# Optimization experiments

Measured on AMD Instinct MI355X. Metric: run time of the kernel, lower is better.

Reference implementation:

```python
import jax, jax.numpy as jnp
import numpy as np

EPS = 1e-5
B, H, W = 128, 98, 40

def _conv2d(x, w):
    return jax.lax.conv_general_dilated(x, w, (1, 1), 'VALID', dimension_numbers=('NCHW', 'OIHW', 'NCHW'))

def _bn_ch(x, g, b):
    # BatchNorm over (B,H,W) per channel (training-mode batch stats, as in the torch default mode)
    m = jnp.mean(x, (0, 2, 3), keepdims=True)
    v = jnp.var(x, (0, 2, 3), keepdims=True)
    return (x - m) * jax.lax.rsqrt(v + EPS) * g[None, :, None, None] + b[None, :, None, None]

def _bn_all(x, g, b):
    # BatchNorm3d(1): single channel -> normalize over the whole tensor
    m = jnp.mean(x)
    v = jnp.var(x)
    return (x - m) * jax.lax.rsqrt(v + EPS) * g[0] + b[0]

def _lc(h, w, b):
    # 62 distinct tiny Conv3d(1,1,(3,1,1)) == locally-connected window-3 conv over channel axis: 64 -> 62
    out = b[None, :, None, None]
    for k in range(3):
        out = out + h[:, k:k + 62] * w[None, :, k, None, None]
    return out

def _lc_block(h, lcw, lcb, gs, bs, Wm, bm, gm, bbm):
    h = jax.nn.relu(_bn_all(_lc(h, lcw, lcb), gs, bs))
    # Conv3d kernel (62,1,1): pure channel mixing 62 -> 64 (no relu after, matching torch code)
    h = jnp.einsum('bdhw,cd->bchw', h, Wm) + bm[None, :, None, None]
    return _bn_ch(h, gm, bbm)

def setup_inputs():
    ks = iter(jax.random.split(jax.random.key(0), 64))
    def rn(shape, s=0.05):
        return jax.random.normal(next(ks), shape, jnp.float32) * s
    d = {}
    d['x'] = jax.random.normal(next(ks), (B, H * 0 + 98 if False else 1, 98, 40), jnp.float32) if False else jax.random.normal(next(ks), (B, 1, H, W), jnp.float32)
    d['W11'] = rn((64, 1, 20, 8)); d['b11'] = rn((64,)); d['g11'] = jnp.ones((64,), jnp.float32); d['be11'] = jnp.zeros((64,), jnp.float32)
    d['lc1_w'] = rn((62, 3), 0.3); d['lc1_b'] = rn((62,)); d['g12'] = jnp.ones((1,), jnp.float32); d['be12'] = jnp.zeros((1,), jnp.float32)
    d['W13'] = rn((64, 62)); d['b13'] = rn((64,)); d['g13'] = jnp.ones((64,), jnp.float32); d['be13'] = jnp.zeros((64,), jnp.float32)
    d['W21'] = rn((64, 64, 15, 8), 0.01); d['b21'] = rn((64,)); d['g21'] = jnp.ones((64,), jnp.float32); d['be21'] = jnp.zeros((64,), jnp.float32)
    d['lc2_w'] = rn((62, 3), 0.3); d['lc2_b'] = rn((62,)); d['g22'] = jnp.ones((1,), jnp.float32); d['be22'] = jnp.zeros((1,), jnp.float32)
    d['W23'] = rn((64, 62)); d['b23'] = rn((64,)); d['g23'] = jnp.ones((64,), jnp.float32); d['be23'] = jnp.zeros((64,), jnp.float32)
    d['W31'] = rn((64, 64, 10, 8), 0.01); d['b31'] = rn((64,)); d['g31'] = jnp.ones((64,), jnp.float32); d['be31'] = jnp.zeros((64,), jnp.float32)
    d['lc3_w'] = rn((62, 3), 0.3); d['lc3_b'] = rn((62,)); d['g32'] = jnp.ones((1,), jnp.float32); d['be32'] = jnp.zeros((1,), jnp.float32)
    d['W33'] = rn((64, 62)); d['b33'] = rn((64,)); d['g33'] = jnp.ones((64,), jnp.float32); d['be33'] = jnp.zeros((64,), jnp.float32)
    d['Wf1'] = rn((64, 64 * 56 * 19), 0.01); d['bf1'] = rn((64,)); d['gf'] = jnp.ones((64,), jnp.float32); d['bef'] = jnp.zeros((64,), jnp.float32)
    d['Wf2'] = rn((35, 64)); d['bf2'] = rn((35,))
    return d

def reference(x, W11, b11, g11, be11, lc1_w, lc1_b, g12, be12, W13, b13, g13, be13, W21, b21, g21, be21, lc2_w, lc2_b, g22, be22, W23, b23, g23, be23, W31, b31, g31, be31, lc3_w, lc3_b, g32, be32, W33, b33, g33, be33, Wf1, bf1, gf, bef, Wf2, bf2):
    h = jax.nn.relu(_bn_ch(_conv2d(x, W11) + b11[None, :, None, None], g11, be11))      # [B,64,79,33]
    h = _lc_block(h, lc1_w, lc1_b, g12, be12, W13, b13, g13, be13)                       # [B,64,79,33]
    h = jax.nn.relu(_bn_ch(_conv2d(h, W21) + b21[None, :, None, None], g21, be21))       # [B,64,65,26]
    h = _lc_block(h, lc2_w, lc2_b, g22, be22, W23, b23, g23, be23)                       # [B,64,65,26]
    h = jax.nn.relu(_bn_ch(_conv2d(h, W31) + b31[None, :, None, None], g31, be31))       # [B,64,56,19]
    h = _lc_block(h, lc3_w, lc3_b, g32, be32, W33, b33, g33, be33)                       # [B,64,56,19]
    h = h.reshape(h.shape[0], -1)                                                        # [B,68096]
    h = h @ Wf1.T + bf1
    m = jnp.mean(h, 0)
    v = jnp.var(h, 0)
    h = jax.nn.relu((h - m) * jax.lax.rsqrt(v + EPS) * gf + bef)
    return h @ Wf2.T + bf2
```

## Files before the change

kernel.cpp:

```cpp
#include <hip/hip_runtime.h>

typedef __bf16 bfrag __attribute__((ext_vector_type(8)));
typedef float ffrag __attribute__((ext_vector_type(16)));

constexpr int Bn  = 128;
constexpr int H0  = 98, Wi0 = 40;
constexpr int KH1 = 20, KW1 = 8, H1 = 79, Wo1 = 33, P1 = H1 * Wo1;
constexpr int KH2 = 15, KW2 = 8, H2 = 65, Wo2 = 26, P2 = H2 * Wo2;
constexpr int KH3 = 10, KW3 = 8, H3 = 56, Wo3 = 19, P3 = H3 * Wo3;
constexpr int M1  = Bn * P1;
constexpr int M2  = Bn * P2;
constexpr int M3  = Bn * P3;
constexpr int KFC = 64 * P3;
constexpr int FCCH = 128;
constexpr int FCKL = KFC / FCCH;
constexpr float EPSF = 1e-5f;

constexpr size_t oA  = 0;
constexpr size_t oB  = oA  + (size_t)Bn * 64 * P1;
constexpr size_t oW2 = oB  + (size_t)Bn * 62 * P1;
constexpr size_t oW3 = oW2 + 245760;
constexpr size_t oW1 = oW3 + 163840;
constexpr size_t oWM = oW1 + 5120;
constexpr size_t oBF = oWM + 6144;
constexpr size_t oP  = oBF + 128;
constexpr size_t oSt = oP  + (size_t)FCCH * 8192;
constexpr size_t oF  = oSt + 9 * 128;

__device__ __forceinline__ float wred(float v) {
    #pragma unroll
    for (int o = 32; o > 0; o >>= 1) v += __shfl_down(v, o);
    return v;
}

constexpr int NZ  = 9 * 128;
constexpr int NW1 = 10240;
constexpr int NWM = 3 * 4096;
constexpr int NPREP = NZ + NW1 + NWM;
__global__ __launch_bounds__(256) void k_prep_all(
    const float* __restrict__ W11, const float* __restrict__ W13,
    const float* __restrict__ W23, const float* __restrict__ W33,
    __bf16* __restrict__ wq1, __bf16* __restrict__ wqm,
    float* __restrict__ st)
{
    int idx = blockIdx.x * 256 + threadIdx.x;
    if (idx < NZ) { st[idx] = 0.f; return; }
    idx -= NZ;
    if (idx < NW1) {
        int j = idx & 7, oc = (idx >> 3) & 63, khh = idx >> 9;
        wq1[idx] = (__bf16)W11[(size_t)oc * 160 + khh * 8 + j];
        return;
    }
    idx -= NW1;
    if (idx < NWM) {
        int which = idx >> 12, r = idx & 4095;
        int j = r & 7, oc = (r >> 3) & 63, sub = (r >> 9) & 1, ks = r >> 10;
        int k = ks * 16 + sub * 8 + j;
        const float* Wm = which == 0 ? W13 : (which == 1 ? W23 : W33);
        wqm[idx] = (k < 62) ? (__bf16)Wm[oc * 62 + k] : (__bf16)0.f;
    }
}

template <int KH, int KW>
__global__ __launch_bounds__(256) void k_foldw(
    const float* __restrict__ W, const float* __restrict__ stp,
    const float* __restrict__ g, const float* __restrict__ be,
    float inv, const float* __restrict__ bias,
    __bf16* __restrict__ wqf, float* __restrict__ biasf)
{
    constexpr int KK = KH * KW;
    __shared__ float sSc[64], sSh[64], ls[4];
    const int t = threadIdx.x;
    if (t < 64) {
        float mm = stp[t] * inv;
        float vv = stp[64 + t] * inv - mm * mm;
        float sc = g[t] * rsqrtf(vv + EPSF);
        sSc[t] = sc;
        sSh[t] = be[t] - mm * sc;
    }
    __syncthreads();
    const int oc = blockIdx.x;
    float local = 0.f;
    for (int i = t; i < 64 * KK; i += 256) {
        int ic = i / KK, rem = i - ic * KK;
        int kh = rem / KW, kw = rem - kh * KW;
        float wv = W[(((size_t)oc * 64 + ic) * KH + kh) * KW + kw];
        int c = ic >> 4, sub = (ic >> 3) & 1, j = ic & 7, pos = kh * KW + kw;
        wqf[(size_t)pos * 4096 + c * 1024 + sub * 512 + oc * 8 + j] = (__bf16)(wv * sSc[ic]);
        local += wv * sSh[ic];
    }
    local = wred(local);
    int wv2 = t >> 6, ln = t & 63;
    if (ln == 0) ls[wv2] = local;
    __syncthreads();
    if (t == 0) biasf[oc] = bias[oc] + ls[0] + ls[1] + ls[2] + ls[3];
}

constexpr int C1COPY = 1736;
__global__ __launch_bounds__(256, 2) void k_conv1m(
    const float* __restrict__ x, const __bf16* __restrict__ wq,
    const float* __restrict__ bias, float* __restrict__ out,
    float* __restrict__ sto)
{
    const int b = blockIdx.y;
    const int m0 = blockIdx.x * 512;
    const int t = threadIdx.x, lane = t & 63, wv = t >> 6;
    const int l31 = lane & 31, lh = lane >> 5;
    __shared__ __align__(16) __bf16 X8[8 * C1COPY];

    const int oh_lo = m0 / Wo1;
    int abase[4];
    #pragma unroll
    for (int mt = 0; mt < 4; ++mt) {
        int m = m0 + wv * 128 + mt * 32 + l31;
        int mc = m > P1 - 1 ? P1 - 1 : m;
        int oh = mc / Wo1, ow = mc - oh * Wo1;
        int s = ow & 7;
        abase[mt] = s * C1COPY + (oh - oh_lo) * 48 + (ow - s);
    }
    for (int idx = t; idx < 8 * 36 * 6; idx += 256) {
        int s = idx / 216; int rr = idx - s * 216;
        int r = rr / 6, q = rr - r * 6;
        int ih = oh_lo + r; if (ih > H0 - 1) ih = H0 - 1;
        const float* src = x + ((size_t)b * H0 + ih) * Wi0;
        __bf16 tmp[8] __attribute__((aligned(16)));
        #pragma unroll
        for (int j = 0; j < 8; ++j) {
            int col = q * 8 + s + j; if (col > Wi0 - 1) col = Wi0 - 1;
            tmp[j] = (__bf16)src[col];
        }
        *(uint4*)&X8[s * C1COPY + r * 48 + q * 8] = *(uint4*)tmp;
    }
    __syncthreads();

    ffrag acc[4][2] = {};
    #pragma unroll 1
    for (int st2 = 0; st2 < 10; ++st2) {
        const int khl = st2 * 2 + lh;
        const __bf16* wp = wq + ((size_t)khl * 64 + l31) * 8;
        bfrag b0 = *(const bfrag*)(wp);
        bfrag b1 = *(const bfrag*)(wp + 256);
        #pragma unroll
        for (int mt = 0; mt < 4; ++mt) {
            bfrag a = *(const bfrag*)&X8[abase[mt] + khl * 48];
            acc[mt][0] = __builtin_amdgcn_mfma_f32_32x32x16_bf16(a, b0, acc[mt][0], 0, 0, 0);
            acc[mt][1] = __builtin_amdgcn_mfma_f32_32x32x16_bf16(a, b1, acc[mt][1], 0, 0, 0);
        }
    }

    float sS[2] = {0.f, 0.f}, sSS[2] = {0.f, 0.f};
    #pragma unroll
    for (int nt = 0; nt < 2; ++nt) {
        int oc = nt * 32 + l31;
        float bv = bias[oc];
        float* op = out + ((size_t)b * 64 + oc) * P1;
        #pragma unroll
        for (int mt = 0; mt < 4; ++mt) {
            int mbase = m0 + wv * 128 + mt * 32 + lh * 4;
            #pragma unroll
            for (int g = 0; g < 4; ++g) {
                int mr = mbase + g * 8;
                float v0 = acc[mt][nt][g * 4 + 0] + bv;
                float v1 = acc[mt][nt][g * 4 + 1] + bv;
                float v2 = acc[mt][nt][g * 4 + 2] + bv;
                float v3 = acc[mt][nt][g * 4 + 3] + bv;
                if (mr + 1 < P1) {
                    *(float2*)(op + mr) = make_float2(v0, v1);
                    sS[nt] += v0 + v1; sSS[nt] += v0 * v0 + v1 * v1;
                    if (mr + 3 < P1) {
                        *(float2*)(op + mr + 2) = make_float2(v2, v3);
                        sS[nt] += v2 + v3; sSS[nt] += v2 * v2 + v3 * v3;
                    } else if (mr + 2 < P1) {
                        op[mr + 2] = v2; sS[nt] += v2; sSS[nt] += v2 * v2;
                    }
                } else if (mr < P1) {
                    op[mr] = v0; sS[nt] += v0; sSS[nt] += v0 * v0;
                }
            }
        }
    }
    #pragma unroll
    for (int nt = 0; nt < 2; ++nt) {
        sS[nt]  += __shfl_down(sS[nt], 32);
        sSS[nt] += __shfl_down(sSS[nt], 32);
    }
    __syncthreads();
    float* redS  = (float*)X8;
    float* redSS = redS + 256;
    if (lane < 32) {
        #pragma unroll
        for (int nt = 0; nt < 2; ++nt) {
            redS[wv * 64 + nt * 32 + l31]  = sS[nt];
            redSS[wv * 64 + nt * 32 + l31] = sSS[nt];
        }
    }
    __syncthreads();
    if (t < 64) {
        atomicAdd(&sto[t],      redS[t] + redS[64 + t] + redS[128 + t] + redS[192 + t]);
        atomicAdd(&sto[64 + t], redSS[t] + redSS[64 + t] + redSS[128 + t] + redSS[192 + t]);
    }
}

template <int POS>
__global__ __launch_bounds__(256) void k_lc(const float* __restrict__ in,
                                            const float* __restrict__ stp,
                                            const float* __restrict__ g,
                                            const float* __restrict__ be,
                                            float inv,
                                            const float* __restrict__ lcw,
                                            const float* __restrict__ lcb,
                                            __bf16* __restrict__ Z,
                                            float* __restrict__ sto) {
    __shared__ float sAff[128];
    __shared__ float sred[4], ssred[4];
    if (threadIdx.x < 64) {
        int tt = threadIdx.x;
        float mm = stp[tt] * inv;
        float vv = stp[64 + tt] * inv - mm * mm;
        float sc = g[tt] * rsqrtf(vv + EPSF);
        sAff[tt] = sc;
        sAff[64 + tt] = be[tt] - mm * sc;
    }
    __syncthreads();
    int morig = blockIdx.x * 256 + threadIdx.x;
    bool valid = morig < Bn * POS;
    int m = valid ? morig : Bn * POS - 1;
    int b = m / POS; int p = m - b * POS;
    const float* ip = in + (size_t)b * 64 * POS + p;
    __bf16 zb[64] __attribute__((aligned(16)));
    zb[62] = (__bf16)0.f; zb[63] = (__bf16)0.f;
    float ts = 0.f, tss = 0.f;
    float y0 = fmaxf(sAff[0] * ip[0]           + sAff[64], 0.f);
    float y1 = fmaxf(sAff[1] * ip[(size_t)POS] + sAff[65], 0.f);
    for (int c = 0; c < 62; ++c) {
        float y2 = fmaxf(sAff[c + 2] * ip[(size_t)(c + 2) * POS] + sAff[64 + c + 2], 0.f);
        float o = lcb[c] + y0 * lcw[c * 3] + y1 * lcw[c * 3 + 1] + y2 * lcw[c * 3 + 2];
        zb[c] = (__bf16)o;
        if (valid) { ts += o; tss += o * o; }
        y0 = y1; y1 = y2;
    }
    __bf16* zp = Z + (size_t)m * 64;
    #pragma unroll
    for (int j = 0; j < 8; ++j)
        *(uint4*)(zp + j * 8) = *(uint4*)(zb + j * 8);
    ts = wred(ts); tss = wred(tss);
    int wv = threadIdx.x >> 6, ln = threadIdx.x & 63;
    if (ln == 0) { sred[wv] = ts; ssred[wv] = tss; }
    __syncthreads();
    if (threadIdx.x == 0) {
        atomicAdd(&sto[0],  sred[0] + sred[1] + sred[2] + sred[3]);
        atomicAdd(&sto[64], ssred[0] + ssred[1] + ssred[2] + ssred[3]);
    }
}

template <int POS, int IH, int IW, bool OUTBF>
__global__ __launch_bounds__(256, 2) void k_mixm(
    const __bf16* __restrict__ Z, const float* __restrict__ stp,
    const float* __restrict__ g, const float* __restrict__ be,
    float inv, const __bf16* __restrict__ wqm,
    const float* __restrict__ bm, void* __restrict__ outv,
    float* __restrict__ sto)
{
    const int b = blockIdx.y;
    const int m0 = blockIdx.x * 512;
    const int t = threadIdx.x, lane = t & 63, wv = t >> 6;
    const int l31 = lane & 31, lh = lane >> 5;

    float mm = stp[0] * inv;
    float vv = stp[64] * inv - mm * mm;
    float s0 = g[0] * rsqrtf(vv + EPSF);
    float t0 = be[0] - mm * s0;

    size_t zbase[4];
    #pragma unroll
    for (int mt = 0; mt < 4; ++mt) {
        int m = m0 + wv * 128 + mt * 32 + l31;
        int mc = m > POS - 1 ? POS - 1 : m;
        zbase[mt] = ((size_t)b * POS + mc) * 64;
    }

    ffrag acc[4][2] = {};
    #pragma unroll
    for (int ks = 0; ks < 4; ++ks) {
        const __bf16* wp = wqm + ks * 1024 + lh * 512 + l31 * 8;
        bfrag b0 = *(const bfrag*)wp;
        bfrag b1 = *(const bfrag*)(wp + 256);
        #pragma unroll
        for (int mt = 0; mt < 4; ++mt) {
            uint4 raw = *(const uint4*)(Z + zbase[mt] + ks * 16 + lh * 8);
            const __bf16* zin = (const __bf16*)&raw;
            __bf16 zout[8] __attribute__((aligned(16)));
            #pragma unroll
            for (int j = 0; j < 8; ++j) {
                float f = (float)zin[j];
                zout[j] = (__bf16)fmaxf(fmaf(s0, f, t0), 0.f);
            }
            bfrag a = *(const bfrag*)zout;
            acc[mt][0] = __builtin_amdgcn_mfma_f32_32x32x16_bf16(a, b0, acc[mt][0], 0, 0, 0);
            acc[mt][1] = __builtin_amdgcn_mfma_f32_32x32x16_bf16(a, b1, acc[mt][1], 0, 0, 0);
        }
    }

    float sS[2] = {0.f, 0.f}, sSS[2] = {0.f, 0.f};
    #pragma unroll
    for (int nt = 0; nt < 2; ++nt) {
        int oc = nt * 32 + l31;
        float bv = bm[oc];
        if constexpr (OUTBF) {
            __bf16* op = (__bf16*)outv;
            #pragma unroll
            for (int mt = 0; mt < 4; ++mt) {
                int mbase = m0 + wv * 128 + mt * 32 + lh * 4;
                #pragma unroll
                for (int g4 = 0; g4 < 4; ++g4) {
                    #pragma unroll
                    for (int q = 0; q < 4; ++q) {
                        int mr = mbase + g4 * 8 + q;
                        if (mr < POS) {
                            float v = acc[mt][nt][g4 * 4 + q] + bv;
                            int ih = mr / IW, iw = mr - ih * IW;
                            op[((size_t)(b * IH + ih) * 2 + nt) * (IW * 32) + iw * 32 + l31] = (__bf16)v;
                            sS[nt] += v; sSS[nt] += v * v;
                        }
                    }
                }
            }
        } else {
            float* op = (float*)outv + ((size_t)b * 64 + oc) * POS;
            #pragma unroll
            for (int mt = 0; mt < 4; ++mt) {
                int mbase = m0 + wv * 128 + mt * 32 + lh * 4;
                #pragma unroll
                for (int g4 = 0; g4 < 4; ++g4) {
                    int mr = mbase + g4 * 8;
                    if (mr < POS) {
                        float v0 = acc[mt][nt][g4 * 4 + 0] + bv;
                        float v1 = acc[mt][nt][g4 * 4 + 1] + bv;
                        *(float2*)(op + mr) = make_float2(v0, v1);
                        sS[nt] += v0 + v1; sSS[nt] += v0 * v0 + v1 * v1;
                        if (mr + 2 < POS) {
                            float v2 = acc[mt][nt][g4 * 4 + 2] + bv;
                            float v3 = acc[mt][nt][g4 * 4 + 3] + bv;
                            *(float2*)(op + mr + 2) = make_float2(v2, v3);
                            sS[nt] += v2 + v3; sSS[nt] += v2 * v2 + v3 * v3;
                        }
                    }
                }
            }
        }
    }
    #pragma unroll
    for (int nt = 0; nt < 2; ++nt) {
        sS[nt]  += __shfl_down(sS[nt], 32);
        sSS[nt] += __shfl_down(sSS[nt], 32);
    }
    __shared__ float red[512];
    if (lane < 32) {
        #pragma unroll
        for (int nt = 0; nt < 2; ++nt) {
            red[wv * 64 + nt * 32 + l31]       = sS[nt];
            red[256 + wv * 64 + nt * 32 + l31] = sSS[nt];
        }
    }
    __syncthreads();
    if (t < 64) {
        atomicAdd(&sto[t],      red[t] + red[64 + t] + red[128 + t] + red[192 + t]);
        atomicAdd(&sto[64 + t], red[256 + t] + red[320 + t] + red[384 + t] + red[448 + t]);
    }
}

template <int KH, int KW, int IH, int IW, int OH, int OW, int NR>
__global__ __launch_bounds__(256, 2) void k_convmfma(
    const __bf16* __restrict__ in,
    const __bf16* __restrict__ wq,
    const float* __restrict__ bias,
    float* __restrict__ out,
    float* __restrict__ sto)
{
    constexpr int P = OH * OW;
    const int b  = blockIdx.y;
    const int m0 = blockIdx.x * 512;
    const int t  = threadIdx.x;
    const int lane = t & 63;
    const int wv = t >> 6;
    const int l31 = lane & 31, lh = lane >> 5;

    __shared__ __align__(16) __bf16 As[NR * IW * 32 + 64];

    const int oh_lo = m0 / OW;
    int posm[4];
    #pragma unroll
    for (int mt = 0; mt < 4; ++mt) {
        int m = m0 + wv * 128 + mt * 32 + l31;
        int mc = m > P - 1 ? P - 1 : m;
        int oh = mc / OW, ow = mc - oh * OW;
        posm[mt] = (oh - oh_lo) * IW + ow;
    }

    ffrag acc[4][2] = {};

    for (int ich = 0; ich < 2; ++ich) {
        __syncthreads();
        constexpr int ROWCH = IW * 4;
        constexpr int CH = NR * ROWCH;
        for (int idx = t; idx < CH; idx += 256) {
            int r = idx / ROWCH, o = idx - r * ROWCH;
            int ih = oh_lo + r; if (ih > IH - 1) ih = IH - 1;
            const __bf16* src = in + ((size_t)(b * IH + ih) * 2 + ich) * (IW * 32) + o * 8;
            int sw = idx ^ ((idx >> 2) & 7);
            *(uint4*)&As[sw * 8] = *(const uint4*)src;
        }
        __syncthreads();

        const __bf16* wich = wq + ich * 2048;
        for (int kh = 0; kh < KH; ++kh) {
            const int rowoff = kh * IW;
            const __bf16* wkh = wich + (size_t)(kh * KW) * 4096 + lh * 512 + l31 * 8;
            #pragma unroll 1
            for (int kw = 0; kw < KW; ++kw) {
                const __bf16* wp = wkh + kw * 4096;
                #pragma unroll
                for (int cc = 0; cc < 2; ++cc) {
                    bfrag b0 = *(const bfrag*)(wp + cc * 1024);
                    bfrag b1 = *(const bfrag*)(wp + cc * 1024 + 256);
                    #pragma unroll
                    for (int mt = 0; mt < 4; ++mt) {
                        int X = posm[mt] + rowoff + kw;
                        int gc = (X << 2) + cc * 2 + lh;
                        bfrag a = *(const bfrag*)&As[(gc ^ (X & 7)) * 8];
                        acc[mt][0] = __builtin_amdgcn_mfma_f32_32x32x16_bf16(a, b0, acc[mt][0], 0, 0, 0);
                        acc[mt][1] = __builtin_amdgcn_mfma_f32_32x32x16_bf16(a, b1, acc[mt][1], 0, 0, 0);
                    }
                }
            }
        }
    }

    float sS[2] = {0.f, 0.f}, sSS[2] = {0.f, 0.f};
    #pragma unroll
    for (int nt = 0; nt < 2; ++nt) {
        int oc = nt * 32 + l31;
        float bv = bias[oc];
        float* op = out + ((size_t)b * 64 + oc) * P;
        #pragma unroll
        for (int mt = 0; mt < 4; ++mt) {
            int mbase = m0 + wv * 128 + mt * 32 + lh * 4;
            #pragma unroll
            for (int g = 0; g < 4; ++g) {
                int mr = mbase + g * 8;
                if (mr < P) {
                    float v0 = acc[mt][nt][g * 4 + 0] + bv;
                    float v1 = acc[mt][nt][g * 4 + 1] + bv;
                    *(float2*)(op + mr) = make_float2(v0, v1);
                    sS[nt] += v0 + v1; sSS[nt] += v0 * v0 + v1 * v1;
                    if (mr + 2 < P) {
                        float v2 = acc[mt][nt][g * 4 + 2] + bv;
                        float v3 = acc[mt][nt][g * 4 + 3] + bv;
                        *(float2*)(op + mr + 2) = make_float2(v2, v3);
                        sS[nt] += v2 + v3; sSS[nt] += v2 * v2 + v3 * v3;
                    }
                }
            }
        }
    }
    #pragma unroll
    for (int nt = 0; nt < 2; ++nt) {
        sS[nt]  += __shfl_down(sS[nt], 32);
        sSS[nt] += __shfl_down(sSS[nt], 32);
    }
    __syncthreads();
    float* redS  = (float*)As;
    float* redSS = redS + 256;
    if (lane < 32) {
        #pragma unroll
        for (int nt = 0; nt < 2; ++nt) {
            redS[wv * 64 + nt * 32 + l31]  = sS[nt];
            redSS[wv * 64 + nt * 32 + l31] = sSS[nt];
        }
    }
    __syncthreads();
    if (t < 64) {
        atomicAdd(&sto[t],      redS[t] + redS[64 + t] + redS[128 + t] + redS[192 + t]);
        atomicAdd(&sto[64 + t], redSS[t] + redSS[64 + t] + redSS[128 + t] + redSS[192 + t]);
    }
}

__global__ __launch_bounds__(256) void k_transpose(const float* __restrict__ in,
                                                   const float* __restrict__ stp,
                                                   const float* __restrict__ g,
                                                   const float* __restrict__ be,
                                                   float inv,
                                                   float* __restrict__ hT) {
    __shared__ float tile[32][33];
    int j0 = blockIdx.x * 32, b0 = blockIdx.y * 32;
    int lo = threadIdx.x & 31, hi = threadIdx.x >> 5;
    int c  = (j0 + lo) / P3;
    float mm = stp[c] * inv;
    float vv = stp[64 + c] * inv - mm * mm;
    float sc = g[c] * rsqrtf(vv + EPSF);
    float sh = be[c] - mm * sc;
    #pragma unroll
    for (int tt = 0; tt < 4; ++tt) {
        int bl = tt * 8 + hi;
        tile[bl][lo] = sc * in[(size_t)(b0 + bl) * KFC + (j0 + lo)] + sh;
    }
    __syncthreads();
    #pragma unroll
    for (int tt = 0; tt < 4; ++tt) {
        int jl = tt * 8 + hi;
        hT[(size_t)(j0 + jl) * Bn + b0 + lo] = tile[lo][jl];
    }
}

__global__ __launch_bounds__(256) void k_fc1(const float* __restrict__ hT,
                                             const float* __restrict__ Wf1,
                                             float* __restrict__ Pb) {
    int lane = threadIdx.x & 63;
    int f0 = __builtin_amdgcn_readfirstlane((threadIdx.x >> 6) * 16);
    int b  = blockIdx.y * 64 + lane;
    int kc = blockIdx.x;
    int k0 = kc * FCKL;
    float acc[16] = {};
    for (int k = k0; k < k0 + FCKL; ++k) {
        float hv = hT[(size_t)k * Bn + b];
        #pragma unroll
        for (int f = 0; f < 16; ++f)
            acc[f] += hv * Wf1[(size_t)(f0 + f) * KFC + k];
    }
    float* pp = Pb + (size_t)kc * 8192 + (size_t)b * 64 + f0;
    #pragma unroll
    for (int f = 0; f < 16; ++f) pp[f] = acc[f];
}

__global__ __launch_bounds__(256) void k_fc1red(const float* __restrict__ Pb,
                                                float* __restrict__ F) {
    int m = blockIdx.x * 256 + threadIdx.x;
    float s = 0.f;
    for (int kc = 0; kc < FCCH; ++kc) s += Pb[(size_t)kc * 8192 + m];
    F[m] = s;
}

__global__ __launch_bounds__(256) void k_fcfin(const float* __restrict__ F,
                                               const float* __restrict__ bf1,
                                               const float* __restrict__ gf,
                                               const float* __restrict__ bef,
                                               const float* __restrict__ Wf2,
                                               const float* __restrict__ bf2,
                                               float* __restrict__ out) {
    __shared__ float sF[8192];
    __shared__ float sfa[128];
    const int t = threadIdx.x;
    for (int m = t; m < 8192; m += 256) sF[m] = F[m];
    __syncthreads();
    if (t < 64) {
        float s = 0.f, ss = 0.f;
        for (int b = 0; b < Bn; ++b) {
            float v = sF[b * 64 + t] + bf1[t];
            s += v; ss += v * v;
        }
        float m  = s / 128.f;
        float va = ss / 128.f - m * m;
        float sc = gf[t] * rsqrtf(va + EPSF);
        sfa[t] = sc;
        sfa[64 + t] = sc * bf1[t] + bef[t] - m * sc;
    }
    __syncthreads();
    for (int m = t; m < Bn * 35; m += 256) {
        int b = m / 35, o = m - b * 35;
        float acc = bf2[o];
        for (int ff = 0; ff < 64; ++ff) {
            int f = (ff + t) & 63;
            float z = fmaxf(sfa[f] * sF[b * 64 + f] + sfa[64 + f], 0.f);
            acc += z * Wf2[o * 64 + f];
        }
        out[m] = acc;
    }
}

extern "C" void kernel_launch(void* const* d_in, const int* in_sizes, int n_in,
                              void* d_out, int out_size, void* d_ws, size_t ws_size,
                              hipStream_t stream) {
    const float* x    = (const float*)d_in[0];
    const float* W11  = (const float*)d_in[1];
    const float* b11  = (const float*)d_in[2];
    const float* g11  = (const float*)d_in[3];
    const float* be11 = (const float*)d_in[4];
    const float* lc1w = (const float*)d_in[5];
    const float* lc1b = (const float*)d_in[6];
    const float* g12  = (const float*)d_in[7];
    const float* be12 = (const float*)d_in[8];
    const float* W13  = (const float*)d_in[9];
    const float* b13  = (const float*)d_in[10];
    const float* g13  = (const float*)d_in[11];
    const float* be13 = (const float*)d_in[12];
    const float* W21  = (const float*)d_in[13];
    const float* b21  = (const float*)d_in[14];
    const float* g21  = (const float*)d_in[15];
    const float* be21 = (const float*)d_in[16];
    const float* lc2w = (const float*)d_in[17];
    const float* lc2b = (const float*)d_in[18];
    const float* g22  = (const float*)d_in[19];
    const float* be22 = (const float*)d_in[20];
    const float* W23  = (const float*)d_in[21];
    const float* b23  = (const float*)d_in[22];
    const float* g23  = (const float*)d_in[23];
    const float* be23 = (const float*)d_in[24];
    const float* W31  = (const float*)d_in[25];
    const float* b31  = (const float*)d_in[26];
    const float* g31  = (const float*)d_in[27];
    const float* be31 = (const float*)d_in[28];
    const float* lc3w = (const float*)d_in[29];
    const float* lc3b = (const float*)d_in[30];
    const float* g32  = (const float*)d_in[31];
    const float* be32 = (const float*)d_in[32];
    const float* W33  = (const float*)d_in[33];
    const float* b33  = (const float*)d_in[34];
    const float* g33  = (const float*)d_in[35];
    const float* be33 = (const float*)d_in[36];
    const float* Wf1  = (const float*)d_in[37];
    const float* bf1  = (const float*)d_in[38];
    const float* gf   = (const float*)d_in[39];
    const float* bef  = (const float*)d_in[40];
    const float* Wf2  = (const float*)d_in[41];
    const float* bf2  = (const float*)d_in[42];

    float* ws  = (float*)d_ws;
    float* A   = ws + oA;
    float* Bb  = ws + oB;
    __bf16* Abf = (__bf16*)(ws + oA);
    __bf16* Bbf = (__bf16*)(ws + oB);
    __bf16* wq2f = (__bf16*)(ws + oW2);
    __bf16* wq3f = (__bf16*)(ws + oW3);
    __bf16* wq1  = (__bf16*)(ws + oW1);
    __bf16* wqm  = (__bf16*)(ws + oWM);
    float* bfold = ws + oBF;
    float* Pb  = ws + oP;
    float* st  = ws + oSt;
    float* F   = ws + oF;

    const int blk1 = (M1 + 255) / 256;
    const int blk2 = M2 / 256;
    const int blk3 = M3 / 256;

    k_prep_all<<<(NPREP + 255) / 256, 256, 0, stream>>>(W11, W13, W23, W33, wq1, wqm, st);

    k_conv1m<<<dim3((P1 + 511) / 512, Bn), 256, 0, stream>>>(x, wq1, b11, A, st + 0 * 128);
    k_lc<P1><<<blk1, 256, 0, stream>>>(A, st + 0 * 128, g11, be11, 1.0f / (float)M1,
                                       lc1w, lc1b, Bbf, st + 1 * 128);
    k_mixm<P1, H1, Wo1, true><<<dim3((P1 + 511) / 512, Bn), 256, 0, stream>>>(
        Bbf, st + 1 * 128, g12, be12, 1.0f / (62.0f * (float)M1),
        wqm + 0 * 4096, b13, (void*)Abf, st + 2 * 128);

    k_foldw<KH2, KW2><<<64, 256, 0, stream>>>(W21, st + 2 * 128, g13, be13,
                                              1.0f / (float)M1, b21, wq2f, bfold + 0);
    k_convmfma<KH2, KW2, H1, Wo1, H2, Wo2, 35>
        <<<dim3((P2 + 511) / 512, Bn), 256, 0, stream>>>(Abf, wq2f, bfold + 0, Bb, st + 3 * 128);
    k_lc<P2><<<blk2, 256, 0, stream>>>(Bb, st + 3 * 128, g21, be21, 1.0f / (float)M2,
                                       lc2w, lc2b, Abf, st + 4 * 128);
    k_mixm<P2, H2, Wo2, true><<<dim3((P2 + 511) / 512, Bn), 256, 0, stream>>>(
        Abf, st + 4 * 128, g22, be22, 1.0f / (62.0f * (float)M2),
        wqm + 1 * 4096, b23, (void*)Bbf, st + 5 * 128);

    k_foldw<KH3, KW3><<<64, 256, 0, stream>>>(W31, st + 5 * 128, g23, be23,
                                              1.0f / (float)M2, b31, wq3f, bfold + 64);
    k_convmfma<KH3, KW3, H2, Wo2, H3, Wo3, 37>
        <<<dim3((P3 + 511) / 512, Bn), 256, 0, stream>>>(Bbf, wq3f, bfold + 64, A, st + 6 * 128);
    k_lc<P3><<<blk3, 256, 0, stream>>>(A, st + 6 * 128, g31, be31, 1.0f / (float)M3,
                                       lc3w, lc3b, Bbf, st + 7 * 128);
    k_mixm<P3, 1, 1, false><<<dim3((P3 + 511) / 512, Bn), 256, 0, stream>>>(
        Bbf, st + 7 * 128, g32, be32, 1.0f / (62.0f * (float)M3),
        wqm + 2 * 4096, b33, (void*)A, st + 8 * 128);

    k_transpose<<<dim3(KFC / 32, Bn / 32), 256, 0, stream>>>(
        A, st + 8 * 128, g33, be33, 1.0f / (float)M3, Bb);
    k_fc1<<<dim3(FCCH, 2), 256, 0, stream>>>(Bb, Wf1, Pb);
    k_fc1red<<<32, 256, 0, stream>>>(Pb, F);
    k_fcfin<<<1, 256, 0, stream>>>(F, bf1, gf, bef, Wf2, bf2, (float*)d_out);
}
```

Measured before the change: 1.068 ms.

## Use bf16 MFMA for FC1, spread BN stat atomics over banks, retile conv3

The scalar fp32 FC1 with its transpose kernel is replaced by a bf16 conversion pass for activations and Wf1, followed by an MFMA-based FC1 split over 112 K-chunks. The per-channel statistics atomics are spread across four banks (and 64 slots for the single-channel LC stats), and readers sum the banks, to reduce atomic contention. The third conv is retuned to 3 M-tiles per wave with smaller blocks, and the kw loop is unrolled by 2. FC1 now uses bf16 inputs, which lowers precision, and a conversion pass over Wf1 is added on every call.

```diff
diff --git a/kernel.cpp b/kernel.cpp
--- a/kernel.cpp
+++ b/kernel.cpp
@@ -12,20 +12,23 @@
 constexpr int M2  = Bn * P2;
 constexpr int M3  = Bn * P3;
 constexpr int KFC = 64 * P3;
-constexpr int FCCH = 128;
+constexpr int FCCH = 112;
 constexpr int FCKL = KFC / FCCH;
+constexpr int FCKS = FCKL / 16;
 constexpr float EPSF = 1e-5f;
 
-constexpr size_t oA  = 0;
-constexpr size_t oB  = oA  + (size_t)Bn * 64 * P1;
-constexpr size_t oW2 = oB  + (size_t)Bn * 62 * P1;
-constexpr size_t oW3 = oW2 + 245760;
-constexpr size_t oW1 = oW3 + 163840;
-constexpr size_t oWM = oW1 + 5120;
-constexpr size_t oBF = oWM + 6144;
-constexpr size_t oP  = oBF + 128;
-constexpr size_t oSt = oP  + (size_t)FCCH * 8192;
-constexpr size_t oF  = oSt + 9 * 128;
+constexpr size_t oA   = 0;
+constexpr size_t oB   = oA  + (size_t)Bn * 64 * P1;
+constexpr size_t oHB  = oB;
+constexpr size_t oWF  = oB  + 4358144;
+constexpr size_t oW2  = oB  + (size_t)Bn * 62 * P1;
+constexpr size_t oW3  = oW2 + 245760;
+constexpr size_t oW1  = oW3 + 163840;
+constexpr size_t oWM  = oW1 + 5120;
+constexpr size_t oBF  = oWM + 6144;
+constexpr size_t oP   = oBF + 128;
+constexpr size_t oSt  = oP  + (size_t)FCCH * 8192;
+constexpr size_t oF   = oSt + 9 * 512;
 
 __device__ __forceinline__ float wred(float v) {
     #pragma unroll
@@ -33,7 +36,11 @@
     return v;
 }
 
-constexpr int NZ  = 9 * 128;
+__device__ __forceinline__ float bank4(const float* stp, int c) {
+    return stp[c] + stp[128 + c] + stp[256 + c] + stp[384 + c];
+}
+
+constexpr int NZ  = 9 * 512;
 constexpr int NW1 = 10240;
 constexpr int NWM = 3 * 4096;
 constexpr int NPREP = NZ + NW1 + NWM;
@@ -72,8 +79,8 @@
     __shared__ float sSc[64], sSh[64], ls[4];
     const int t = threadIdx.x;
     if (t < 64) {
-        float mm = stp[t] * inv;
-        float vv = stp[64 + t] * inv - mm * mm;
+        float mm = bank4(stp, t) * inv;
+        float vv = bank4(stp, 64 + t) * inv - mm * mm;
         float sc = g[t] * rsqrtf(vv + EPSF);
         sSc[t] = sc;
         sSh[t] = be[t] - mm * sc;
@@ -196,8 +203,9 @@
     }
     __syncthreads();
     if (t < 64) {
-        atomicAdd(&sto[t],      redS[t] + redS[64 + t] + redS[128 + t] + redS[192 + t]);
-        atomicAdd(&sto[64 + t], redSS[t] + redSS[64 + t] + redSS[128 + t] + redSS[192 + t]);
+        int bank = ((blockIdx.x ^ blockIdx.y) & 3) * 128;
+        atomicAdd(&sto[bank + t],      redS[t] + redS[64 + t] + redS[128 + t] + redS[192 + t]);
+        atomicAdd(&sto[bank + 64 + t], redSS[t] + redSS[64 + t] + redSS[128 + t] + redSS[192 + t]);
     }
 }
 
@@ -215,8 +223,8 @@
     __shared__ float sred[4], ssred[4];
     if (threadIdx.x < 64) {
         int tt = threadIdx.x;
-        float mm = stp[tt] * inv;
-        float vv = stp[64 + tt] * inv - mm * mm;
+        float mm = bank4(stp, tt) * inv;
+        float vv = bank4(stp, 64 + tt) * inv - mm * mm;
         float sc = g[tt] * rsqrtf(vv + EPSF);
         sAff[tt] = sc;
         sAff[64 + tt] = be[tt] - mm * sc;
@@ -248,8 +256,9 @@
     if (ln == 0) { sred[wv] = ts; ssred[wv] = tss; }
     __syncthreads();
     if (threadIdx.x == 0) {
-        atomicAdd(&sto[0],  sred[0] + sred[1] + sred[2] + sred[3]);
-        atomicAdd(&sto[64], ssred[0] + ssred[1] + ssred[2] + ssred[3]);
+        int slot = blockIdx.x & 63;
+        atomicAdd(&sto[slot],      sred[0] + sred[1] + sred[2] + sred[3]);
+        atomicAdd(&sto[64 + slot], ssred[0] + ssred[1] + ssred[2] + ssred[3]);
     }
 }
 
@@ -266,8 +275,11 @@
     const int t = threadIdx.x, lane = t & 63, wv = t >> 6;
     const int l31 = lane & 31, lh = lane >> 5;
 
-    float mm = stp[0] * inv;
-    float vv = stp[64] * inv - mm * mm;
+    float gs = 0.f, gss = 0.f;
+    #pragma unroll
+    for (int i = 0; i < 64; ++i) { gs += stp[i]; gss += stp[64 + i]; }
+    float mm = gs * inv;
+    float vv = gss * inv - mm * mm;
     float s0 = g[0] * rsqrtf(vv + EPSF);
     float t0 = be[0] - mm * s0;
 
@@ -364,12 +376,13 @@
     }
     __syncthreads();
     if (t < 64) {
-        atomicAdd(&sto[t],      red[t] + red[64 + t] + red[128 + t] + red[192 + t]);
-        atomicAdd(&sto[64 + t], red[256 + t] + red[320 + t] + red[384 + t] + red[448 + t]);
-    }
-}
-
-template <int KH, int KW, int IH, int IW, int OH, int OW, int NR>
+        int bank = ((blockIdx.x ^ blockIdx.y) & 3) * 128;
+        atomicAdd(&sto[bank + t],      red[t] + red[64 + t] + red[128 + t] + red[192 + t]);
+        atomicAdd(&sto[bank + 64 + t], red[256 + t] + red[320 + t] + red[384 + t] + red[448 + t]);
+    }
+}
+
+template <int KH, int KW, int IH, int IW, int OH, int OW, int NR, int MT>
 __global__ __launch_bounds__(256, 2) void k_convmfma(
     const __bf16* __restrict__ in,
     const __bf16* __restrict__ wq,
@@ -378,8 +391,9 @@
     float* __restrict__ sto)
 {
     constexpr int P = OH * OW;
+    constexpr int MB = 128 * MT;
     const int b  = blockIdx.y;
-    const int m0 = blockIdx.x * 512;
+    const int m0 = blockIdx.x * MB;
     const int t  = threadIdx.x;
     const int lane = t & 63;
     const int wv = t >> 6;
@@ -388,16 +402,16 @@
     __shared__ __align__(16) __bf16 As[NR * IW * 32 + 64];
 
     const int oh_lo = m0 / OW;
-    int posm[4];
-    #pragma unroll
-    for (int mt = 0; mt < 4; ++mt) {
-        int m = m0 + wv * 128 + mt * 32 + l31;
+    int posm[MT];
+    #pragma unroll
+    for (int mt = 0; mt < MT; ++mt) {
+        int m = m0 + wv * (32 * MT) + mt * 32 + l31;
         int mc = m > P - 1 ? P - 1 : m;
         int oh = mc / OW, ow = mc - oh * OW;
         posm[mt] = (oh - oh_lo) * IW + ow;
     }
 
-    ffrag acc[4][2] = {};
+    ffrag acc[MT][2] = {};
 
     for (int ich = 0; ich < 2; ++ich) {
         __syncthreads();
@@ -416,7 +430,7 @@
         for (int kh = 0; kh < KH; ++kh) {
             const int rowoff = kh * IW;
             const __bf16* wkh = wich + (size_t)(kh * KW) * 4096 + lh * 512 + l31 * 8;
-            #pragma unroll 1
+            #pragma unroll 2
             for (int kw = 0; kw < KW; ++kw) {
                 const __bf16* wp = wkh + kw * 4096;
                 #pragma unroll
@@ -424,7 +438,7 @@
                     bfrag b0 = *(const bfrag*)(wp + cc * 1024);
                     bfrag b1 = *(const bfrag*)(wp + cc * 1024 + 256);
                     #pragma unroll
-                    for (int mt = 0; mt < 4; ++mt) {
+                    for (int mt = 0; mt < MT; ++mt) {
                         int X = posm[mt] + rowoff + kw;
                         int gc = (X << 2) + cc * 2 + lh;
                         bfrag a = *(const bfrag*)&As[(gc ^ (X & 7)) * 8];
@@ -443,8 +457,8 @@
         float bv = bias[oc];
         float* op = out + ((size_t)b * 64 + oc) * P;
         #pragma unroll
-        for (int mt = 0; mt < 4; ++mt) {
-            int mbase = m0 + wv * 128 + mt * 32 + lh * 4;
+        for (int mt = 0; mt < MT; ++mt) {
+            int mbase = m0 + wv * (32 * MT) + mt * 32 + lh * 4;
             #pragma unroll
             for (int g = 0; g < 4; ++g) {
                 int mr = mbase + g * 8;
@@ -480,56 +494,80 @@
     }
     __syncthreads();
     if (t < 64) {
-        atomicAdd(&sto[t],      redS[t] + redS[64 + t] + redS[128 + t] + redS[192 + t]);
-        atomicAdd(&sto[64 + t], redSS[t] + redSS[64 + t] + redSS[128 + t] + redSS[192 + t]);
-    }
-}
-
-__global__ __launch_bounds__(256) void k_transpose(const float* __restrict__ in,
-                                                   const float* __restrict__ stp,
-                                                   const float* __restrict__ g,
-                                                   const float* __restrict__ be,
-                                                   float inv,
-                                                   float* __restrict__ hT) {
-    __shared__ float tile[32][33];
-    int j0 = blockIdx.x * 32, b0 = blockIdx.y * 32;
-    int lo = threadIdx.x & 31, hi = threadIdx.x >> 5;
-    int c  = (j0 + lo) / P3;
-    float mm = stp[c] * inv;
-    float vv = stp[64 + c] * inv - mm * mm;
-    float sc = g[c] * rsqrtf(vv + EPSF);
-    float sh = be[c] - mm * sc;
-    #pragma unroll
-    for (int tt = 0; tt < 4; ++tt) {
-        int bl = tt * 8 + hi;
-        tile[bl][lo] = sc * in[(size_t)(b0 + bl) * KFC + (j0 + lo)] + sh;
-    }
-    __syncthreads();
-    #pragma unroll
-    for (int tt = 0; tt < 4; ++tt) {
-        int jl = tt * 8 + hi;
-        hT[(size_t)(j0 + jl) * Bn + b0 + lo] = tile[lo][jl];
-    }
-}
-
-__global__ __launch_bounds__(256) void k_fc1(const float* __restrict__ hT,
-                                             const float* __restrict__ Wf1,
-                                             float* __restrict__ Pb) {
-    int lane = threadIdx.x & 63;
-    int f0 = __builtin_amdgcn_readfirstlane((threadIdx.x >> 6) * 16);
-    int b  = blockIdx.y * 64 + lane;
-    int kc = blockIdx.x;
-    int k0 = kc * FCKL;
-    float acc[16] = {};
-    for (int k = k0; k < k0 + FCKL; ++k) {
-        float hv = hT[(size_t)k * Bn + b];
-        #pragma unroll
-        for (int f = 0; f < 16; ++f)
-            acc[f] += hv * Wf1[(size_t)(f0 + f) * KFC + k];
-    }
-    float* pp = Pb + (size_t)kc * 8192 + (size_t)b * 64 + f0;
-    #pragma unroll
-    for (int f = 0; f < 16; ++f) pp[f] = acc[f];
+        int bank = ((blockIdx.x ^ blockIdx.y) & 3) * 128;
+        atomicAdd(&sto[bank + t],      redS[t] + redS[64 + t] + redS[128 + t] + redS[192 + t]);
+        atomicAdd(&sto[bank + 64 + t], redSS[t] + redSS[64 + t] + redSS[128 + t] + redSS[192 + t]);
+    }
+}
+
+constexpr int NHB  = M3 * 64 / 8;
+constexpr int NWFB = 64 * KFC / 8;
+__global__ __launch_bounds__(256) void k_prep_hb(
+    const float* __restrict__ Y, const float* __restrict__ stp,
+    const float* __restrict__ g, const float* __restrict__ be, float inv,
+    const float* __restrict__ Wf1,
+    __bf16* __restrict__ hb, __bf16* __restrict__ wf1b)
+{
+    int idx = blockIdx.x * 256 + threadIdx.x;
+    if (idx < NHB) {
+        size_t base = (size_t)idx * 8;
+        int c = (int)(base / P3) & 63;
+        float mm = bank4(stp, c) * inv;
+        float vv = bank4(stp, 64 + c) * inv - mm * mm;
+        float sc = g[c] * rsqrtf(vv + EPSF);
+        float sh = be[c] - mm * sc;
+        __bf16 tmp[8] __attribute__((aligned(16)));
+        #pragma unroll
+        for (int j = 0; j < 8; ++j)
+            tmp[j] = (__bf16)(sc * Y[base + j] + sh);
+        *(uint4*)(hb + base) = *(uint4*)tmp;
+        return;
+    }
+    idx -= NHB;
+    if (idx < NWFB) {
+        size_t base = (size_t)idx * 8;
+        __bf16 tmp[8] __attribute__((aligned(16)));
+        #pragma unroll
+        for (int j = 0; j < 8; ++j)
+            tmp[j] = (__bf16)Wf1[base + j];
+        *(uint4*)(wf1b + base) = *(uint4*)tmp;
+    }
+}
+
+__global__ __launch_bounds__(256) void k_fc1m(const __bf16* __restrict__ hb,
+                                              const __bf16* __restrict__ wf1b,
+                                              float* __restrict__ Pb) {
+    const int kc = blockIdx.x;
+    const int t = threadIdx.x, lane = t & 63, wv = t >> 6;
+    const int l31 = lane & 31, lh = lane >> 5;
+    const int k0 = kc * FCKL;
+
+    const __bf16* ap = hb + (size_t)(wv * 32 + l31) * KFC + k0 + lh * 8;
+    const __bf16* bp0 = wf1b + (size_t)l31 * KFC + k0 + lh * 8;
+    const __bf16* bp1 = wf1b + (size_t)(32 + l31) * KFC + k0 + lh * 8;
+
+    ffrag acc[2] = {};
+    #pragma unroll 2
+    for (int ks = 0; ks < FCKS; ++ks) {
+        bfrag a  = *(const bfrag*)(ap  + ks * 16);
+        bfrag b0 = *(const bfrag*)(bp0 + ks * 16);
+        bfrag b1 = *(const bfrag*)(bp1 + ks * 16);
+        acc[0] = __builtin_amdgcn_mfma_f32_32x32x16_bf16(a, b0, acc[0], 0, 0, 0);
+        acc[1] = __builtin_amdgcn_mfma_f32_32x32x16_bf16(a, b1, acc[1], 0, 0, 0);
+    }
+    float* pp = Pb + (size_t)kc * 8192;
+    #pragma unroll
+    for (int nt = 0; nt < 2; ++nt) {
+        #pragma unroll
+        for (int g = 0; g < 4; ++g) {
+            #pragma unroll
+            for (int q = 0; q < 4; ++q) {
+                int row = q + g * 8 + lh * 4;
+                int bb = wv * 32 + row;
+                pp[bb * 64 + nt * 32 + l31] = acc[nt][g * 4 + q];
+            }
+        }
+    }
 }
 
 __global__ __launch_bounds__(256) void k_fc1red(const float* __restrict__ Pb,
@@ -629,6 +667,8 @@
     float* Bb  = ws + oB;
     __bf16* Abf = (__bf16*)(ws + oA);
     __bf16* Bbf = (__bf16*)(ws + oB);
+    __bf16* hb   = (__bf16*)(ws + oHB);
+    __bf16* wf1b = (__bf16*)(ws + oWF);
     __bf16* wq2f = (__bf16*)(ws + oW2);
     __bf16* wq3f = (__bf16*)(ws + oW3);
     __bf16* wq1  = (__bf16*)(ws + oW1);
@@ -644,36 +684,36 @@
 
     k_prep_all<<<(NPREP + 255) / 256, 256, 0, stream>>>(W11, W13, W23, W33, wq1, wqm, st);
 
-    k_conv1m<<<dim3((P1 + 511) / 512, Bn), 256, 0, stream>>>(x, wq1, b11, A, st + 0 * 128);
-    k_lc<P1><<<blk1, 256, 0, stream>>>(A, st + 0 * 128, g11, be11, 1.0f / (float)M1,
-                                       lc1w, lc1b, Bbf, st + 1 * 128);
+    k_conv1m<<<dim3((P1 + 511) / 512, Bn), 256, 0, stream>>>(x, wq1, b11, A, st + 0 * 512);
+    k_lc<P1><<<blk1, 256, 0, stream>>>(A, st + 0 * 512, g11, be11, 1.0f / (float)M1,
+                                       lc1w, lc1b, Bbf, st + 1 * 512);
     k_mixm<P1, H1, Wo1, true><<<dim3((P1 + 511) / 512, Bn), 256, 0, stream>>>(
-        Bbf, st + 1 * 128, g12, be12, 1.0f / (62.0f * (float)M1),
-        wqm + 0 * 4096, b13, (void*)Abf, st + 2 * 128);
-
-    k_foldw<KH2, KW2><<<64, 256, 0, stream>>>(W21, st + 2 * 128, g13, be13,
+        Bbf, st + 1 * 512, g12, be12, 1.0f / (62.0f * (float)M1),
+        wqm + 0 * 4096, b13, (void*)Abf, st + 2 * 512);
+
+    k_foldw<KH2, KW2><<<64, 256, 0, stream>>>(W21, st + 2 * 512, g13, be13,
                                               1.0f / (float)M1, b21, wq2f, bfold + 0);
-    k_convmfma<KH2, KW2, H1, Wo1, H2, Wo2, 35>
-        <<<dim3((P2 + 511) / 512, Bn), 256, 0, stream>>>(Abf, wq2f, bfold + 0, Bb, st + 3 * 128);
-    k_lc<P2><<<blk2, 256, 0, stream>>>(Bb, st + 3 * 128, g21, be21, 1.0f / (float)M2,
-                                       lc2w, lc2b, Abf, st + 4 * 128);
+    k_convmfma<KH2, KW2, H1, Wo1, H2, Wo2, 35, 4>
+        <<<dim3((P2 + 511) / 512, Bn), 256, 0, stream>>>(Abf, wq2f, bfold + 0, Bb, st + 3 * 512);
+    k_lc<P2><<<blk2, 256, 0, stream>>>(Bb, st + 3 * 512, g21, be21, 1.0f / (float)M2,
+                                       lc2w, lc2b, Abf, st + 4 * 512);
     k_mixm<P2, H2, Wo2, true><<<dim3((P2 + 511) / 512, Bn), 256, 0, stream>>>(
-        Abf, st + 4 * 128, g22, be22, 1.0f / (62.0f * (float)M2),
-        wqm + 1 * 4096, b23, (void*)Bbf, st + 5 * 128);
-
-    k_foldw<KH3, KW3><<<64, 256, 0, stream>>>(W31, st + 5 * 128, g23, be23,
+        Abf, st + 4 * 512, g22, be22, 1.0f / (62.0f * (float)M2),
+        wqm + 1 * 4096, b23, (void*)Bbf, st + 5 * 512);
+
+    k_foldw<KH3, KW3><<<64, 256, 0, stream>>>(W31, st + 5 * 512, g23, be23,
                                               1.0f / (float)M2, b31, wq3f, bfold + 64);
-    k_convmfma<KH3, KW3, H2, Wo2, H3, Wo3, 37>
-        <<<dim3((P3 + 511) / 512, Bn), 256, 0, stream>>>(Bbf, wq3f, bfold + 64, A, st + 6 * 128);
-    k_lc<P3><<<blk3, 256, 0, stream>>>(A, st + 6 * 128, g31, be31, 1.0f / (float)M3,
-                                       lc3w, lc3b, Bbf, st + 7 * 128);
+    k_convmfma<KH3, KW3, H2, Wo2, H3, Wo3, 30, 3>
+        <<<dim3((P3 + 383) / 384, Bn), 256, 0, stream>>>(Bbf, wq3f, bfold + 64, A, st + 6 * 512);
+    k_lc<P3><<<blk3, 256, 0, stream>>>(A, st + 6 * 512, g31, be31, 1.0f / (float)M3,
+                                       lc3w, lc3b, Bbf, st + 7 * 512);
     k_mixm<P3, 1, 1, false><<<dim3((P3 + 511) / 512, Bn), 256, 0, stream>>>(
-        Bbf, st + 7 * 128, g32, be32, 1.0f / (62.0f * (float)M3),
-        wqm + 2 * 4096, b33, (void*)A, st + 8 * 128);
-
-    k_transpose<<<dim3(KFC / 32, Bn / 32), 256, 0, stream>>>(
-        A, st + 8 * 128, g33, be33, 1.0f / (float)M3, Bb);
-    k_fc1<<<dim3(FCCH, 2), 256, 0, stream>>>(Bb, Wf1, Pb);
+        Bbf, st + 7 * 512, g32, be32, 1.0f / (62.0f * (float)M3),
+        wqm + 2 * 4096, b33, (void*)A, st + 8 * 512);
+
+    k_prep_hb<<<(NHB + NWFB + 255) / 256, 256, 0, stream>>>(
+        A, st + 8 * 512, g33, be33, 1.0f / (float)M3, Wf1, hb, wf1b);
+    k_fc1m<<<FCCH, 256, 0, stream>>>(hb, wf1b, Pb);
     k_fc1red<<<32, 256, 0, stream>>>(Pb, F);
     k_fcfin<<<1, 256, 0, stream>>>(F, bf1, gf, bef, Wf2, bf2, (float*)d_out);
 }
```

After: 909.6 us. 1.17x faster.
